# Optimization experiments

Measured on AMD Instinct MI355X. Metric: run time of the kernel, lower is better.

The kernel has to match this reference:

```python
import jax, jax.numpy as jnp
import numpy as np

N_NODES = 16384
HIDDEN = 512
INPUT = 512
MAX_CHILDREN = 4


def _build_tree(n, k, seed=0):
    """Random forest where every child index < parent index (topological order)."""
    rng = np.random.default_rng(seed)
    parent = np.minimum(np.arange(n - 1) + 1 + rng.integers(1, 16, size=n - 1), n - 1)
    child_idx = np.zeros((n, k), dtype=np.int32)
    cnt = np.zeros(n, dtype=np.int32)
    for j in range(n - 1):
        p = int(parent[j])
        if cnt[p] < k:
            child_idx[p, cnt[p]] = j
            cnt[p] += 1
    child_mask = (np.arange(k)[None, :] < cnt[:, None]).astype(np.int32)
    return child_idx, child_mask


def setup_inputs() -> dict:
    key = jax.random.key(0)
    ks = jax.random.split(key, 8)
    s_in = 1.0 / np.sqrt(INPUT)
    s_h = 1.0 / np.sqrt(HIDDEN)
    child_idx, child_mask = _build_tree(N_NODES, MAX_CHILDREN)
    return {
        "inputs": jax.random.normal(ks[0], (N_NODES, INPUT), jnp.float32),
        "i2h_weight": jax.random.uniform(ks[1], (4 * HIDDEN, INPUT), jnp.float32, -s_in, s_in),
        "i2h_bias": jax.random.uniform(ks[2], (4 * HIDDEN,), jnp.float32, -s_in, s_in),
        "hs2h_weight": jax.random.uniform(ks[3], (3 * HIDDEN, HIDDEN), jnp.float32, -s_h, s_h),
        "hs2h_bias": jax.random.uniform(ks[4], (3 * HIDDEN,), jnp.float32, -s_h, s_h),
        "hc2h_weight": jax.random.uniform(ks[5], (HIDDEN, HIDDEN), jnp.float32, -s_h, s_h),
        "hc2h_bias": jax.random.uniform(ks[6], (HIDDEN,), jnp.float32, -s_h, s_h),
        "child_idx": jnp.asarray(child_idx),
        "child_mask": jnp.asarray(child_mask),
    }


def reference(inputs, i2h_weight, i2h_bias, hs2h_weight, hs2h_bias,
              hc2h_weight, hc2h_bias, child_idx, child_mask):
    n, _ = inputs.shape
    hid = hc2h_weight.shape[0]
    # Batched input projection for all nodes at once: [N, 4H]
    i2h = inputs @ i2h_weight.T + i2h_bias
    i2h_i, i2h_f, i2h_u, i2h_o = jnp.split(i2h, 4, axis=1)
    i2h_iuo = jnp.concatenate([i2h_i, i2h_u, i2h_o], axis=1)  # [N, 3H]
    cmask = child_mask.astype(inputs.dtype)                    # [N, K]

    def step(carry, xs):
        H, C = carry
        idx, iuo_pre, f_pre, cidx, m = xs
        hc = H[cidx]                                  # [K, H] gathered child h
        cc = C[cidx]                                  # [K, H] gathered child c
        mm = m[:, None]
        hs = jnp.sum(hc * mm, axis=0)                 # child-sum h: [H]
        # per-child forget gate: sigmoid(W_x x + b_f + h_k @ W_hc)
        f = jax.nn.sigmoid(f_pre + hc2h_bias + hc @ hc2h_weight)  # [K, H]
        fc = jnp.sum(f * cc * mm, axis=0)             # [H]
        iuo = iuo_pre + hs @ hs2h_weight.T + hs2h_bias  # [3H]
        i_g, u_g, o_g = jnp.split(iuo, 3)
        next_c = jax.nn.sigmoid(i_g) * jnp.tanh(u_g) + fc
        next_h = jax.nn.sigmoid(o_g) * jnp.tanh(next_c)
        return (H.at[idx].set(next_h), C.at[idx].set(next_c)), None

    H0 = jnp.zeros((n, hid), inputs.dtype)
    C0 = jnp.zeros((n, hid), inputs.dtype)
    (H, C), _ = jax.lax.scan(step, (H0, C0),
                             (jnp.arange(n), i2h_iuo, i2h_f, child_idx, cmask))
    return jnp.stack([H, C])  # [2, N, H]: next_h and next_c for every node
```

## Files before the change

kernel.cpp:

```cpp
#include <hip/hip_runtime.h>
#include <math.h>

#define N_NODES 16384
#define HID 512
#define G4 2048
#define MAXC 4

#define T_TEAMS 16
#define S_WGS 16
#define NWG 256
#define BLK 512
#define NSUB 16
#define ECH 32
#define FPN 16

#define AT_LD(p)    __hip_atomic_load((p), __ATOMIC_RELAXED, __HIP_MEMORY_SCOPE_AGENT)
#define AT_ST(p, v) __hip_atomic_store((p), (v), __ATOMIC_RELAXED, __HIP_MEMORY_SCOPE_AGENT)

__device__ __forceinline__ float sigm(float x) { return 1.0f / (1.0f + __expf(-x)); }

#define BK 16
__global__ void __launch_bounds__(256) gemm_i2h(
    const float* __restrict__ A, const float* __restrict__ B,
    const float* __restrict__ bias, float* __restrict__ C)
{
  __shared__ float As[BK][68];
  __shared__ float Bs[BK][68];
  const int tid = threadIdx.x;
  const int tx = tid & 15, ty = tid >> 4;
  const int rowBase = blockIdx.y * 64, colBase = blockIdx.x * 64;
  const int r = tid >> 2;
  const int kk = (tid & 3) << 2;
  float acc[4][4] = {};

  for (int k0 = 0; k0 < 512; k0 += BK) {
    float4 a4 = *(const float4*)&A[(size_t)(rowBase + r) * 512 + k0 + kk];
    float4 b4 = *(const float4*)&B[(size_t)(colBase + r) * 512 + k0 + kk];
    __syncthreads();
    As[kk + 0][r] = a4.x; As[kk + 1][r] = a4.y; As[kk + 2][r] = a4.z; As[kk + 3][r] = a4.w;
    Bs[kk + 0][r] = b4.x; Bs[kk + 1][r] = b4.y; Bs[kk + 2][r] = b4.z; Bs[kk + 3][r] = b4.w;
    __syncthreads();
#pragma unroll
    for (int k = 0; k < BK; k++) {
      float4 av = *(const float4*)&As[k][ty << 2];
      float4 bv = *(const float4*)&Bs[k][tx << 2];
      float a0 = av.x, a1 = av.y, a2 = av.z, a3 = av.w;
      float b0 = bv.x, b1 = bv.y, b2 = bv.z, b3 = bv.w;
      acc[0][0] += a0 * b0; acc[0][1] += a0 * b1; acc[0][2] += a0 * b2; acc[0][3] += a0 * b3;
      acc[1][0] += a1 * b0; acc[1][1] += a1 * b1; acc[1][2] += a1 * b2; acc[1][3] += a1 * b3;
      acc[2][0] += a2 * b0; acc[2][1] += a2 * b1; acc[2][2] += a2 * b2; acc[2][3] += a2 * b3;
      acc[3][0] += a3 * b0; acc[3][1] += a3 * b1; acc[3][2] += a3 * b2; acc[3][3] += a3 * b3;
    }
  }
#pragma unroll
  for (int i = 0; i < 4; i++) {
    const int row = rowBase + (ty << 2) + i;
    const int col = colBase + (tx << 2);
    float4 o;
    o.x = acc[i][0] + bias[col + 0];
    o.y = acc[i][1] + bias[col + 1];
    o.z = acc[i][2] + bias[col + 2];
    o.w = acc[i][3] + bias[col + 3];
    *(float4*)&C[(size_t)row * G4 + col] = o;
  }
}

template<int NC>
__device__ __forceinline__ void gates_lds(
    const float (*hch)[HID], int e0,
    const float4* wi, const float4* wu, const float4* wo, const float* wf,
    float& aI, float& aU, float& aO, float (&aF)[4])
{
#pragma unroll
  for (int q = 0; q < 8; q++) {
    float4 c0 = *(const float4*)&hch[0][e0 + 4 * q];
    float4 c1 = {0,0,0,0}, c2 = {0,0,0,0}, c3 = {0,0,0,0};
    if constexpr (NC > 1) c1 = *(const float4*)&hch[1][e0 + 4 * q];
    if constexpr (NC > 2) c2 = *(const float4*)&hch[2][e0 + 4 * q];
    if constexpr (NC > 3) c3 = *(const float4*)&hch[3][e0 + 4 * q];
    float sx = c0.x, sy = c0.y, sz = c0.z, sw = c0.w;
    if constexpr (NC > 1) { sx += c1.x; sy += c1.y; sz += c1.z; sw += c1.w; }
    if constexpr (NC > 2) { sx += c2.x; sy += c2.y; sz += c2.z; sw += c2.w; }
    if constexpr (NC > 3) { sx += c3.x; sy += c3.y; sz += c3.z; sw += c3.w; }
    aI += wi[q].x * sx; aI += wi[q].y * sy; aI += wi[q].z * sz; aI += wi[q].w * sw;
    aU += wu[q].x * sx; aU += wu[q].y * sy; aU += wu[q].z * sz; aU += wu[q].w * sw;
    aO += wo[q].x * sx; aO += wo[q].y * sy; aO += wo[q].z * sz; aO += wo[q].w * sw;
    aF[0] += wf[4*q+0] * c0.x; aF[0] += wf[4*q+1] * c0.y;
    aF[0] += wf[4*q+2] * c0.z; aF[0] += wf[4*q+3] * c0.w;
    if constexpr (NC > 1) {
      aF[1] += wf[4*q+0] * c1.x; aF[1] += wf[4*q+1] * c1.y;
      aF[1] += wf[4*q+2] * c1.z; aF[1] += wf[4*q+3] * c1.w;
    }
    if constexpr (NC > 2) {
      aF[2] += wf[4*q+0] * c2.x; aF[2] += wf[4*q+1] * c2.y;
      aF[2] += wf[4*q+2] * c2.z; aF[2] += wf[4*q+3] * c2.w;
    }
    if constexpr (NC > 3) {
      aF[3] += wf[4*q+0] * c3.x; aF[3] += wf[4*q+1] * c3.y;
      aF[3] += wf[4*q+2] * c3.z; aF[3] += wf[4*q+3] * c3.w;
    }
  }
}

__global__ void __launch_bounds__(BLK, 2) recur(
    const float* __restrict__ i2h,
    const float* __restrict__ hs2h_w, const float* __restrict__ hc2h_w,
    const float* __restrict__ hs2h_b, const float* __restrict__ hc2h_b,
    const int* __restrict__ child_idx, const int* __restrict__ child_mask,
    float* Hout, float* Cout, int* flags)
{
  __shared__ float hch[MAXC][HID];
  __shared__ float red[7][NSUB][32];

  const int tid = threadIdx.x;
  const int wg = blockIdx.x;
  const int team = wg & (T_TEAMS - 1);
  const int slice = wg >> 4;
  const int rr = tid & 31;
  const int sub = tid >> 5;
  const int rp = slice * 32 + rr;
  const int e0 = sub * ECH;

  float4 wi[8], wu[8], wo[8];
  float wf[32];
#pragma unroll
  for (int q = 0; q < 8; q++) {
    wi[q] = *(const float4*)&hs2h_w[(size_t)rp * HID + e0 + 4 * q];
    wu[q] = *(const float4*)&hs2h_w[(size_t)(512 + rp) * HID + e0 + 4 * q];
    wo[q] = *(const float4*)&hs2h_w[(size_t)(1024 + rp) * HID + e0 + 4 * q];
  }
#pragma unroll
  for (int e = 0; e < 32; e++)
    wf[e] = hc2h_w[(size_t)(e0 + e) * HID + rp];

  const int rpp = slice * 32 + tid;
  float bI = 0.f, bU = 0.f, bO = 0.f, bF = 0.f;
  if (tid < 32) {
    bI = hs2h_b[rpp]; bU = hs2h_b[512 + rpp];
    bO = hs2h_b[1024 + rpp]; bF = hc2h_b[rpp];
  }

  for (int j = team; j < N_NODES; j += T_TEAMS) {
    const int4 ci = *(const int4*)&child_idx[j * 4];
    const int4 cm = *(const int4*)&child_mask[j * 4];
    const int nc = cm.x + cm.y + cm.z + cm.w;
    const int cix[4] = {ci.x, ci.y, ci.z, ci.w};

    float ipre = 0.f, fpre = 0.f, upre = 0.f, opre = 0.f;
    if (tid < 32) {
      const size_t jb = (size_t)j * G4;
      ipre = i2h[jb + rpp];
      fpre = i2h[jb + 512 + rpp];
      upre = i2h[jb + 1024 + rpp];
      opre = i2h[jb + 1536 + rpp];
    }

    float aI = 0.f, aU = 0.f, aO = 0.f, aF[4] = {0.f, 0.f, 0.f, 0.f};
    float cC[4] = {0.f, 0.f, 0.f, 0.f};

    if (nc > 0) {
      if (tid < 64) {
        const int k = tid >> 4, s = tid & 15;
        const int cj = (k < nc) ? cix[k] : cix[0];
        int* fp = flags + cj * FPN + s;
        for (;;) {
          const int v = AT_LD(fp);
          const bool ok = (k >= nc) || (v != 0);
          if (__ballot(ok) == ~0ull) break;
        }
      }
      __syncthreads();

#pragma unroll
      for (int k = 0; k < MAXC; k++)
        if (k < nc) hch[k][tid] = AT_LD(Hout + (size_t)cix[k] * HID + tid);
      if (tid < 32) {
#pragma unroll
        for (int k = 0; k < MAXC; k++)
          if (k < nc) cC[k] = AT_LD(Cout + (size_t)cix[k] * HID + rpp);
      }
      __syncthreads();

      switch (nc) {
        case 1: gates_lds<1>(hch, e0, wi, wu, wo, wf, aI, aU, aO, aF); break;
        case 2: gates_lds<2>(hch, e0, wi, wu, wo, wf, aI, aU, aO, aF); break;
        case 3: gates_lds<3>(hch, e0, wi, wu, wo, wf, aI, aU, aO, aF); break;
        default: gates_lds<4>(hch, e0, wi, wu, wo, wf, aI, aU, aO, aF); break;
      }
      red[0][sub][rr] = aI;    red[1][sub][rr] = aU;    red[2][sub][rr] = aO;
      red[3][sub][rr] = aF[0]; red[4][sub][rr] = aF[1];
      red[5][sub][rr] = aF[2]; red[6][sub][rr] = aF[3];
      __syncthreads();
    }

    if (tid < 32) {
      float sI = 0.f, sU = 0.f, sO = 0.f;
      float sF0 = 0.f, sF1 = 0.f, sF2 = 0.f, sF3 = 0.f;
      if (nc > 0) {
#pragma unroll
        for (int s = 0; s < NSUB; s++) {
          sI += red[0][s][tid]; sU += red[1][s][tid]; sO += red[2][s][tid];
          sF0 += red[3][s][tid]; sF1 += red[4][s][tid];
          sF2 += red[5][s][tid]; sF3 += red[6][s][tid];
        }
      }
      const float ig = ipre + bI + sI;
      const float ug = upre + bU + sU;
      const float og = opre + bO + sO;
      float c = sigm(ig) * tanhf(ug);
      if (nc > 0) c += sigm(fpre + bF + sF0) * cC[0];
      if (nc > 1) c += sigm(fpre + bF + sF1) * cC[1];
      if (nc > 2) c += sigm(fpre + bF + sF2) * cC[2];
      if (nc > 3) c += sigm(fpre + bF + sF3) * cC[3];
      const float h = sigm(og) * tanhf(c);
      AT_ST(Hout + (size_t)j * HID + rpp, h);
      AT_ST(Cout + (size_t)j * HID + rpp, c);
    }
    asm volatile("" ::: "memory");
    __builtin_amdgcn_s_waitcnt(0);
    asm volatile("" ::: "memory");
    if (tid == 0)
      AT_ST(flags + j * FPN + slice, 1);
  }
}

extern "C" void kernel_launch(void* const* d_in, const int* in_sizes, int n_in,
                              void* d_out, int out_size, void* d_ws, size_t ws_size,
                              hipStream_t stream) {
  const float* inputs    = (const float*)d_in[0];
  const float* i2h_w     = (const float*)d_in[1];
  const float* i2h_b     = (const float*)d_in[2];
  const float* hs2h_w    = (const float*)d_in[3];
  const float* hs2h_b    = (const float*)d_in[4];
  const float* hc2h_w    = (const float*)d_in[5];
  const float* hc2h_b    = (const float*)d_in[6];
  const int*   child_idx = (const int*)d_in[7];
  const int*   child_mask= (const int*)d_in[8];

  float* Hout = (float*)d_out;
  float* Cout = Hout + (size_t)N_NODES * HID;

  char* ws = (char*)d_ws;
  const size_t i2h_bytes = (size_t)N_NODES * G4 * sizeof(float);
  float* i2h = (float*)ws;
  int*   flags = (int*)(ws + i2h_bytes);

  hipMemsetAsync(flags, 0, N_NODES * FPN * sizeof(int), stream);

  dim3 ggrid(G4 / 64, N_NODES / 64);
  gemm_i2h<<<ggrid, 256, 0, stream>>>(inputs, i2h_w, i2h_b, i2h);
  recur<<<NWG, BLK, 0, stream>>>(i2h, hs2h_w, hc2h_w, hs2h_b, hc2h_b,
                                 child_idx, child_mask, Hout, Cout, flags);
}
```

Before: 8.306 ms.

## Replace per-slice ready flags with sentinel-valued H data polling

Drops the separate flags array. H output is prefilled with an all-ones NaN sentinel, and consumers spin directly on each child's H element until it is no longer the sentinel, storing C before H with a waitcnt between them. This removes one flag round-trip and one barrier per node, packs the reduction into float4 LDS stores, and adds a fast path for leaf nodes. The risk is per-element polling traffic and a correctness dependence on store ordering and on h never equalling the sentinel bit pattern.

```diff
diff --git a/kernel.cpp b/kernel.cpp
--- a/kernel.cpp
+++ b/kernel.cpp
@@ -1,5 +1,6 @@
 #include <hip/hip_runtime.h>
 #include <math.h>
+#include <stdint.h>
 
 #define N_NODES 16384
 #define HID 512
@@ -12,10 +13,12 @@
 #define BLK 512
 #define NSUB 16
 #define ECH 32
-#define FPN 16
-
-#define AT_LD(p)    __hip_atomic_load((p), __ATOMIC_RELAXED, __HIP_MEMORY_SCOPE_AGENT)
-#define AT_ST(p, v) __hip_atomic_store((p), (v), __ATOMIC_RELAXED, __HIP_MEMORY_SCOPE_AGENT)
+
+#define SENT 0xFFFFFFFFu
+
+#define AT_LDF(p)   __hip_atomic_load((p), __ATOMIC_RELAXED, __HIP_MEMORY_SCOPE_AGENT)
+#define AT_LDU(p)   __hip_atomic_load((p), __ATOMIC_RELAXED, __HIP_MEMORY_SCOPE_AGENT)
+#define AT_STF(p,v) __hip_atomic_store((p), (v), __ATOMIC_RELAXED, __HIP_MEMORY_SCOPE_AGENT)
 
 __device__ __forceinline__ float sigm(float x) { return 1.0f / (1.0f + __expf(-x)); }
 
@@ -107,10 +110,12 @@
     const float* __restrict__ hs2h_w, const float* __restrict__ hc2h_w,
     const float* __restrict__ hs2h_b, const float* __restrict__ hc2h_b,
     const int* __restrict__ child_idx, const int* __restrict__ child_mask,
-    float* Hout, float* Cout, int* flags)
+    float* Hout, float* Cout)
 {
   __shared__ float hch[MAXC][HID];
-  __shared__ float red[7][NSUB][32];
+  __shared__ float chc[MAXC][32];
+  __shared__ float4 redA[NSUB][32];
+  __shared__ float4 redB[NSUB][32];
 
   const int tid = threadIdx.x;
   const int wg = blockIdx.x;
@@ -120,6 +125,7 @@
   const int sub = tid >> 5;
   const int rp = slice * 32 + rr;
   const int e0 = sub * ECH;
+  const int lr = tid - slice * 32;
 
   float4 wi[8], wu[8], wo[8];
   float wf[32];
@@ -156,30 +162,28 @@
     }
 
     float aI = 0.f, aU = 0.f, aO = 0.f, aF[4] = {0.f, 0.f, 0.f, 0.f};
-    float cC[4] = {0.f, 0.f, 0.f, 0.f};
 
     if (nc > 0) {
-      if (tid < 64) {
-        const int k = tid >> 4, s = tid & 15;
-        const int cj = (k < nc) ? cix[k] : cix[0];
-        int* fp = flags + cj * FPN + s;
-        for (;;) {
-          const int v = AT_LD(fp);
-          const bool ok = (k >= nc) || (v != 0);
-          if (__ballot(ok) == ~0ull) break;
+#pragma unroll
+      for (int k = 0; k < MAXC; k++) {
+        if (k < nc) {
+          const uint32_t* hp = (const uint32_t*)(Hout + (size_t)cix[k] * HID + tid);
+          uint32_t v = AT_LDU(hp);
+          while (v == SENT) { __builtin_amdgcn_s_sleep(1); v = AT_LDU(hp); }
+          hch[k][tid] = __uint_as_float(v);
+          if ((unsigned)lr < 32u)
+            chc[k][lr] = AT_LDF(Cout + (size_t)cix[k] * HID + tid);
         }
       }
       __syncthreads();
 
-#pragma unroll
-      for (int k = 0; k < MAXC; k++)
-        if (k < nc) hch[k][tid] = AT_LD(Hout + (size_t)cix[k] * HID + tid);
+      float cC0 = 0.f, cC1 = 0.f, cC2 = 0.f, cC3 = 0.f;
       if (tid < 32) {
-#pragma unroll
-        for (int k = 0; k < MAXC; k++)
-          if (k < nc) cC[k] = AT_LD(Cout + (size_t)cix[k] * HID + rpp);
-      }
-      __syncthreads();
+        cC0 = chc[0][tid];
+        if (nc > 1) cC1 = chc[1][tid];
+        if (nc > 2) cC2 = chc[2][tid];
+        if (nc > 3) cC3 = chc[3][tid];
+      }
 
       switch (nc) {
         case 1: gates_lds<1>(hch, e0, wi, wu, wo, wf, aI, aU, aO, aF); break;
@@ -187,40 +191,49 @@
         case 3: gates_lds<3>(hch, e0, wi, wu, wo, wf, aI, aU, aO, aF); break;
         default: gates_lds<4>(hch, e0, wi, wu, wo, wf, aI, aU, aO, aF); break;
       }
-      red[0][sub][rr] = aI;    red[1][sub][rr] = aU;    red[2][sub][rr] = aO;
-      red[3][sub][rr] = aF[0]; red[4][sub][rr] = aF[1];
-      red[5][sub][rr] = aF[2]; red[6][sub][rr] = aF[3];
+      redA[sub][rr] = make_float4(aI, aU, aO, aF[0]);
+      redB[sub][rr] = make_float4(aF[1], aF[2], aF[3], 0.f);
       __syncthreads();
-    }
-
-    if (tid < 32) {
-      float sI = 0.f, sU = 0.f, sO = 0.f;
-      float sF0 = 0.f, sF1 = 0.f, sF2 = 0.f, sF3 = 0.f;
-      if (nc > 0) {
+
+      if (tid < 32) {
+        float sI = 0.f, sU = 0.f, sO = 0.f;
+        float sF0 = 0.f, sF1 = 0.f, sF2 = 0.f, sF3 = 0.f;
 #pragma unroll
         for (int s = 0; s < NSUB; s++) {
-          sI += red[0][s][tid]; sU += red[1][s][tid]; sO += red[2][s][tid];
-          sF0 += red[3][s][tid]; sF1 += red[4][s][tid];
-          sF2 += red[5][s][tid]; sF3 += red[6][s][tid];
+          float4 a = redA[s][tid];
+          float4 b = redB[s][tid];
+          sI += a.x; sU += a.y; sO += a.z; sF0 += a.w;
+          sF1 += b.x; sF2 += b.y; sF3 += b.z;
         }
-      }
-      const float ig = ipre + bI + sI;
-      const float ug = upre + bU + sU;
-      const float og = opre + bO + sO;
-      float c = sigm(ig) * tanhf(ug);
-      if (nc > 0) c += sigm(fpre + bF + sF0) * cC[0];
-      if (nc > 1) c += sigm(fpre + bF + sF1) * cC[1];
-      if (nc > 2) c += sigm(fpre + bF + sF2) * cC[2];
-      if (nc > 3) c += sigm(fpre + bF + sF3) * cC[3];
-      const float h = sigm(og) * tanhf(c);
-      AT_ST(Hout + (size_t)j * HID + rpp, h);
-      AT_ST(Cout + (size_t)j * HID + rpp, c);
-    }
-    asm volatile("" ::: "memory");
-    __builtin_amdgcn_s_waitcnt(0);
-    asm volatile("" ::: "memory");
-    if (tid == 0)
-      AT_ST(flags + j * FPN + slice, 1);
+        const float ig = ipre + bI + sI;
+        const float ug = upre + bU + sU;
+        const float og = opre + bO + sO;
+        float c = sigm(ig) * tanhf(ug);
+        c += sigm(fpre + bF + sF0) * cC0;
+        if (nc > 1) c += sigm(fpre + bF + sF1) * cC1;
+        if (nc > 2) c += sigm(fpre + bF + sF2) * cC2;
+        if (nc > 3) c += sigm(fpre + bF + sF3) * cC3;
+        const float h = sigm(og) * tanhf(c);
+        AT_STF(Cout + (size_t)j * HID + rpp, c);
+        asm volatile("" ::: "memory");
+        __builtin_amdgcn_s_waitcnt(0);
+        asm volatile("" ::: "memory");
+        AT_STF(Hout + (size_t)j * HID + rpp, h);
+      }
+    } else {
+      if (tid < 32) {
+        const float ig = ipre + bI;
+        const float ug = upre + bU;
+        const float og = opre + bO;
+        const float c = sigm(ig) * tanhf(ug);
+        const float h = sigm(og) * tanhf(c);
+        AT_STF(Cout + (size_t)j * HID + rpp, c);
+        asm volatile("" ::: "memory");
+        __builtin_amdgcn_s_waitcnt(0);
+        asm volatile("" ::: "memory");
+        AT_STF(Hout + (size_t)j * HID + rpp, h);
+      }
+    }
   }
 }
 
@@ -240,15 +253,12 @@
   float* Hout = (float*)d_out;
   float* Cout = Hout + (size_t)N_NODES * HID;
 
-  char* ws = (char*)d_ws;
-  const size_t i2h_bytes = (size_t)N_NODES * G4 * sizeof(float);
-  float* i2h = (float*)ws;
-  int*   flags = (int*)(ws + i2h_bytes);
-
-  hipMemsetAsync(flags, 0, N_NODES * FPN * sizeof(int), stream);
+  float* i2h = (float*)d_ws;
+
+  hipMemsetAsync(Hout, 0xFF, (size_t)N_NODES * HID * sizeof(float), stream);
 
   dim3 ggrid(G4 / 64, N_NODES / 64);
   gemm_i2h<<<ggrid, 256, 0, stream>>>(inputs, i2h_w, i2h_b, i2h);
   recur<<<NWG, BLK, 0, stream>>>(i2h, hs2h_w, hc2h_w, hs2h_b, hc2h_b,
-                                 child_idx, child_mask, Hout, Cout, flags);
-}
+                                 child_idx, child_mask, Hout, Cout);
+}
```

New measurement: 9.352 ms. 12.6% more time.
